# Performance work log

Measured on AMD Instinct MI355X. Metric: run time of the kernel, lower is better.

Reference implementation:

```python
import jax, jax.numpy as jnp
import numpy as np

DIM = 14                     # input feature dim == log2(codebook_size)
NUM_CODEBOOKS = 1
CODEBOOK_DIM = DIM           # codebook_dim = log2(2**dim) = dim
CODEBOOK_SIZE = 2 ** DIM     # 16384
DIVERSITY_GAMMA = 1.0
ENTROPY_LOSS_WEIGHT = 0.1
COMMITMENT_LOSS_WEIGHT = 0.25
INV_TEMPERATURE = 100.0
EPS = 1e-5


def _entropy(p):
    # -sum p log p over last dim
    return -(p * jnp.log(jnp.clip(p, EPS))).sum(-1)


def _codebook():
    # all sign codes: bit j of code i -> +/-1, MSB-first mask 2**(d-1..0)
    codes = jnp.arange(CODEBOOK_SIZE, dtype=jnp.int32)[:, None]
    shifts = jnp.arange(CODEBOOK_DIM - 1, -1, -1, dtype=jnp.int32)
    bits = (codes >> shifts) & 1                       # [cs, d]
    return (bits * 2 - 1).astype(jnp.float32)          # [cs, d]


def setup_inputs() -> dict:
    key = jax.random.key(0)
    k1, k2, k3, k4, k5 = jax.random.split(key, 5)
    b, n = 4, 2048
    cdims = CODEBOOK_DIM * NUM_CODEBOOKS
    s = 1.0 / np.sqrt(DIM)
    return {
        "x": jax.random.normal(k1, (b, n, DIM), dtype=jnp.float32),
        "W_in": jax.random.uniform(k2, (cdims, DIM), jnp.float32, -s, s),
        "b_in": jax.random.uniform(k3, (cdims,), jnp.float32, -s, s),
        "W_out": jax.random.uniform(k4, (DIM, cdims), jnp.float32, -s, s),
        "b_out": jax.random.uniform(k5, (DIM,), jnp.float32, -s, s),
    }


def reference(x, W_in, b_in, W_out, b_out):
    b, n, _ = x.shape
    codebook = _codebook()                              # [cs, d]

    h = x @ W_in.T + b_in                               # [b, n, c*d]
    h = h.reshape(b, n, NUM_CODEBOOKS, CODEBOOK_DIM)    # [b, n, c, d]
    original_input = h

    # sign quantization (codebook_scale = 1.0)
    quantized = jnp.where(h > 0, 1.0, -1.0)
    # straight-through estimator (activation = identity)
    h_st = h + jax.lax.stop_gradient(quantized - h)

    # bitmask -> integer indices, MSB-first
    bit_mask = (2 ** jnp.arange(CODEBOOK_DIM - 1, -1, -1)).astype(jnp.int32)
    indices = ((h_st > 0).astype(jnp.int32) * bit_mask).sum(-1)  # [b, n, c]

    # entropy aux loss: prob over all 2**d codes
    # -distance = 2 * <orig, code>; softmax((-distance) * inv_temp)
    logits = (2.0 * INV_TEMPERATURE) * jnp.einsum(
        "bncd,jd->bncj", original_input, codebook)      # [b, n, c, cs]
    prob = jax.nn.softmax(logits, axis=-1)
    prob_flat = prob.reshape(b * n, NUM_CODEBOOKS, CODEBOOK_SIZE)

    per_sample_entropy = _entropy(prob_flat).mean()
    avg_prob = prob_flat.mean(0)                        # [c, cs]
    codebook_entropy = _entropy(avg_prob).mean()
    entropy_aux_loss = per_sample_entropy - DIVERSITY_GAMMA * codebook_entropy

    commit_loss = jnp.mean(
        (original_input - jax.lax.stop_gradient(quantized)) ** 2)

    out = h_st.reshape(b, n, NUM_CODEBOOKS * CODEBOOK_DIM) @ W_out.T + b_out

    indices = indices.squeeze(-1)  # keep_num_codebooks_dim False (c == 1)
    aux_loss = (entropy_aux_loss * ENTROPY_LOSS_WEIGHT
                + commit_loss * COMMITMENT_LOSS_WEIGHT)
    return out, indices, aux_loss
```

## Files before the change

kernel.cpp:

```cpp
#include <hip/hip_runtime.h>
#include <hip/hip_bf16.h>

#define NS 8192
#define D 14
#define CS 16384
#define EPS 1e-5f
#define LNEPS (-11.512925464970229f)
#define THRESH 30.0f

__global__ __launch_bounds__(256) void lfq_zero(float* __restrict__ hist)
{
    ((float4*)hist)[blockIdx.x * 256 + threadIdx.x] =
        make_float4(0.f, 0.f, 0.f, 0.f);
}

__global__ __launch_bounds__(64) void lfq_main(
    const float* __restrict__ x, const float* __restrict__ Win,
    const float* __restrict__ bin, const float* __restrict__ Wout,
    const float* __restrict__ bout,
    float* __restrict__ out, float* __restrict__ idxOut,
    float* __restrict__ hist, float* __restrict__ entPart,
    float* __restrict__ commitPart)
{
    const int tid = threadIdx.x;
    const int i = blockIdx.x * 64 + tid;

    float xv[D];
    #pragma unroll
    for (int k = 0; k < D; k++) xv[k] = x[i * D + k];

    float h[D];
    #pragma unroll
    for (int d = 0; d < D; d++) {
        float s = bin[d];
        #pragma unroll
        for (int k = 0; k < D; k++) s = fmaf(xv[k], Win[d * D + k], s);
        h[d] = s;
    }

    float q[D];
    int idx = 0;
    float commit = 0.f;
    #pragma unroll
    for (int d = 0; d < D; d++) {
        const bool pos = h[d] > 0.f;
        q[d] = pos ? 1.f : -1.f;
        idx |= (pos ? 1 : 0) << (13 - d);
        const float e = h[d] - q[d];
        commit = fmaf(e, e, commit);
    }

    #pragma unroll
    for (int e = 0; e < D; e++) {
        float s = bout[e];
        #pragma unroll
        for (int d = 0; d < D; d++) s = fmaf(q[d], Wout[e * D + d], s);
        out[i * D + e] = s;
    }
    idxOut[i] = (float)idx;

    __shared__ float sA[D * 64];
    __shared__ int   sB[D * 64];
    int S = 0;
    float t0 = 0.f;
    #pragma unroll
    for (int d = 0; d < D; d++) {
        const float ab = fabsf(200.0f * h[d]);
        t0 -= __logf(1.0f + __expf(-2.f * ab));
        const float twoA = 2.f * ab;
        if (twoA < THRESH) {
            sA[S * 64 + tid] = twoA;
            sB[S * 64 + tid] = 1 << (13 - d);
            S++;
        }
    }

    float ent;
    {
        const float p0 = __expf(t0);
        ent = p0 * fmaxf(t0, LNEPS);
        atomicAdd(&hist[idx], p0);
    }
    float tcur = t0;
    int jj = idx;
    const int total = 1 << S;
    for (int m = 1; m < total; m++) {
        const int k = __ffs(m) - 1;
        const int gn = m ^ (m >> 1);
        const float tw = sA[k * 64 + tid];
        const int bm = sB[k * 64 + tid];
        tcur += ((gn >> k) & 1) ? -tw : tw;
        jj ^= bm;
        const float p = __expf(tcur);
        ent = fmaf(p, fmaxf(tcur, LNEPS), ent);
        atomicAdd(&hist[jj], p);
    }

    __shared__ float red[64];
    red[tid] = commit;
    __syncthreads();
    #pragma unroll
    for (int s = 32; s > 0; s >>= 1) {
        if (tid < s) red[tid] += red[tid + s];
        __syncthreads();
    }
    if (tid == 0) commitPart[blockIdx.x] = red[0];
    __syncthreads();
    red[tid] = ent;
    __syncthreads();
    #pragma unroll
    for (int s = 32; s > 0; s >>= 1) {
        if (tid < s) red[tid] += red[tid + s];
        __syncthreads();
    }
    if (tid == 0) entPart[blockIdx.x] = red[0];
}

__global__ __launch_bounds__(256) void lfq_r1(
    const float* __restrict__ hist, float* __restrict__ cbPart)
{
    const int t = threadIdx.x;
    const float4 v = ((const float4*)hist)[blockIdx.x * 256 + t];
    float cb = 0.f;
    #pragma unroll
    for (int u = 0; u < 4; u++) {
        const float qv = (&v.x)[u] * (1.0f / NS);
        cb += qv * __logf(fmaxf(qv, EPS));
    }
    __shared__ float r[256];
    r[t] = cb;
    __syncthreads();
    #pragma unroll
    for (int s = 128; s > 0; s >>= 1) {
        if (t < s) r[t] += r[t + s];
        __syncthreads();
    }
    if (t == 0) cbPart[blockIdx.x] = r[0];
}

__global__ __launch_bounds__(256) void lfq_r2(
    const float* __restrict__ cbPart, const float* __restrict__ entPart,
    const float* __restrict__ commitPart, float* __restrict__ aux)
{
    const int t = threadIdx.x;
    float cb = (t < 16) ? cbPart[t] : 0.f;
    float es = (t < 128) ? entPart[t] : 0.f;
    float cm = (t < 128) ? commitPart[t] : 0.f;

    __shared__ float r1[256], r2[256], r3[256];
    r1[t] = cb; r2[t] = es; r3[t] = cm;
    __syncthreads();
    #pragma unroll
    for (int s = 128; s > 0; s >>= 1) {
        if (t < s) { r1[t] += r1[t + s]; r2[t] += r2[t + s]; r3[t] += r3[t + s]; }
        __syncthreads();
    }
    if (t == 0) {
        const float codebook_entropy = -r1[0];
        const float per_sample_entropy = -r2[0] / (float)NS;
        const float commit_loss = r3[0] / (float)(NS * D);
        const float entropy_aux = per_sample_entropy - 1.0f * codebook_entropy;
        aux[0] = entropy_aux * 0.1f + commit_loss * 0.25f;
    }
}

extern "C" void kernel_launch(void* const* d_in, const int* in_sizes, int n_in,
                              void* d_out, int out_size, void* d_ws, size_t ws_size,
                              hipStream_t stream) {
    const float* x    = (const float*)d_in[0];
    const float* Win  = (const float*)d_in[1];
    const float* bin  = (const float*)d_in[2];
    const float* Wout = (const float*)d_in[3];
    const float* bout = (const float*)d_in[4];

    float* out    = (float*)d_out;
    float* idxOut = out + (size_t)NS * D;
    float* aux    = idxOut + NS;

    float* ws         = (float*)d_ws;
    float* hist       = ws;
    float* entPart    = hist + CS;
    float* commitPart = entPart + 128;
    float* cbPart     = commitPart + 128;

    lfq_zero<<<16, 256, 0, stream>>>(hist);
    lfq_main<<<NS / 64, 64, 0, stream>>>(x, Win, bin, Wout, bout,
                                         out, idxOut, hist, entPart, commitPart);
    lfq_r1<<<16, 256, 0, stream>>>(hist, cbPart);
    lfq_r2<<<1, 256, 0, stream>>>(cbPart, entPart, commitPart, aux);
}
```

Before: 27.78 us.

## Fuse four LFQ kernels into one cooperative kernel with grid syncs

Replaces the zero, main, and two reduction kernels with a single cooperative launch that zeroes the histogram, computes per-sample work, and uses grid.sync barriers before the histogram accumulation and the final reduction. Block reductions switch from shared-memory trees to wave shuffles. This removes three kernel launches and the gaps between them. In exchange, the final codebook-entropy pass over the 16K-entry histogram runs on a single 64-thread block, and the grid barriers add their own cost.

```diff
diff --git a/kernel.cpp b/kernel.cpp
--- a/kernel.cpp
+++ b/kernel.cpp
@@ -1,29 +1,38 @@
 #include <hip/hip_runtime.h>
-#include <hip/hip_bf16.h>
+#include <hip/hip_cooperative_groups.h>
+
+namespace cg = cooperative_groups;
 
 #define NS 8192
 #define D 14
 #define CS 16384
+#define NB 128
+#define BT 64
 #define EPS 1e-5f
 #define LNEPS (-11.512925464970229f)
 #define THRESH 30.0f
 
-__global__ __launch_bounds__(256) void lfq_zero(float* __restrict__ hist)
-{
-    ((float4*)hist)[blockIdx.x * 256 + threadIdx.x] =
-        make_float4(0.f, 0.f, 0.f, 0.f);
+__device__ __forceinline__ float waveRedSum(float v) {
+    #pragma unroll
+    for (int off = 32; off; off >>= 1) v += __shfl_xor(v, off);
+    return v;
 }
 
-__global__ __launch_bounds__(64) void lfq_main(
+__global__ __launch_bounds__(BT) void lfq_all(
     const float* __restrict__ x, const float* __restrict__ Win,
     const float* __restrict__ bin, const float* __restrict__ Wout,
     const float* __restrict__ bout,
     float* __restrict__ out, float* __restrict__ idxOut,
     float* __restrict__ hist, float* __restrict__ entPart,
-    float* __restrict__ commitPart)
+    float* __restrict__ commitPart, float* __restrict__ aux)
 {
+    cg::grid_group grid = cg::this_grid();
     const int tid = threadIdx.x;
-    const int i = blockIdx.x * 64 + tid;
+    const int b = blockIdx.x;
+    const int i = b * BT + tid;
+
+    atomicExch(&hist[2 * i], 0.f);
+    atomicExch(&hist[2 * i + 1], 0.f);
 
     float xv[D];
     #pragma unroll
@@ -59,8 +68,8 @@
     }
     idxOut[i] = (float)idx;
 
-    __shared__ float sA[D * 64];
-    __shared__ int   sB[D * 64];
+    __shared__ float sA[D * BT];
+    __shared__ int   sB[D * BT];
     int S = 0;
     float t0 = 0.f;
     #pragma unroll
@@ -69,11 +78,16 @@
         t0 -= __logf(1.0f + __expf(-2.f * ab));
         const float twoA = 2.f * ab;
         if (twoA < THRESH) {
-            sA[S * 64 + tid] = twoA;
-            sB[S * 64 + tid] = 1 << (13 - d);
+            sA[S * BT + tid] = twoA;
+            sB[S * BT + tid] = 1 << (13 - d);
             S++;
         }
     }
+
+    const float cm = waveRedSum(commit);
+    if (tid == 0) atomicExch(&commitPart[b], cm);
+
+    grid.sync();
 
     float ent;
     {
@@ -87,8 +101,8 @@
     for (int m = 1; m < total; m++) {
         const int k = __ffs(m) - 1;
         const int gn = m ^ (m >> 1);
-        const float tw = sA[k * 64 + tid];
-        const int bm = sB[k * 64 + tid];
+        const float tw = sA[k * BT + tid];
+        const int bm = sB[k * BT + tid];
         tcur += ((gn >> k) & 1) ? -tw : tw;
         jj ^= bm;
         const float p = __expf(tcur);
@@ -96,71 +110,34 @@
         atomicAdd(&hist[jj], p);
     }
 
-    __shared__ float red[64];
-    red[tid] = commit;
-    __syncthreads();
-    #pragma unroll
-    for (int s = 32; s > 0; s >>= 1) {
-        if (tid < s) red[tid] += red[tid + s];
-        __syncthreads();
-    }
-    if (tid == 0) commitPart[blockIdx.x] = red[0];
-    __syncthreads();
-    red[tid] = ent;
-    __syncthreads();
-    #pragma unroll
-    for (int s = 32; s > 0; s >>= 1) {
-        if (tid < s) red[tid] += red[tid + s];
-        __syncthreads();
-    }
-    if (tid == 0) entPart[blockIdx.x] = red[0];
-}
+    const float es = waveRedSum(ent);
+    if (tid == 0) atomicExch(&entPart[b], es);
 
-__global__ __launch_bounds__(256) void lfq_r1(
-    const float* __restrict__ hist, float* __restrict__ cbPart)
-{
-    const int t = threadIdx.x;
-    const float4 v = ((const float4*)hist)[blockIdx.x * 256 + t];
-    float cb = 0.f;
-    #pragma unroll
-    for (int u = 0; u < 4; u++) {
-        const float qv = (&v.x)[u] * (1.0f / NS);
-        cb += qv * __logf(fmaxf(qv, EPS));
-    }
-    __shared__ float r[256];
-    r[t] = cb;
-    __syncthreads();
-    #pragma unroll
-    for (int s = 128; s > 0; s >>= 1) {
-        if (t < s) r[t] += r[t + s];
-        __syncthreads();
-    }
-    if (t == 0) cbPart[blockIdx.x] = r[0];
-}
+    grid.sync();
 
-__global__ __launch_bounds__(256) void lfq_r2(
-    const float* __restrict__ cbPart, const float* __restrict__ entPart,
-    const float* __restrict__ commitPart, float* __restrict__ aux)
-{
-    const int t = threadIdx.x;
-    float cb = (t < 16) ? cbPart[t] : 0.f;
-    float es = (t < 128) ? entPart[t] : 0.f;
-    float cm = (t < 128) ? commitPart[t] : 0.f;
-
-    __shared__ float r1[256], r2[256], r3[256];
-    r1[t] = cb; r2[t] = es; r3[t] = cm;
-    __syncthreads();
-    #pragma unroll
-    for (int s = 128; s > 0; s >>= 1) {
-        if (t < s) { r1[t] += r1[t + s]; r2[t] += r2[t + s]; r3[t] += r3[t + s]; }
-        __syncthreads();
-    }
-    if (t == 0) {
-        const float codebook_entropy = -r1[0];
-        const float per_sample_entropy = -r2[0] / (float)NS;
-        const float commit_loss = r3[0] / (float)(NS * D);
-        const float entropy_aux = per_sample_entropy - 1.0f * codebook_entropy;
-        aux[0] = entropy_aux * 0.1f + commit_loss * 0.25f;
+    if (b == 0) {
+        float cb = 0.f;
+        const float4* h4 = (const float4*)hist;
+        for (int u = 0; u < 64; u++) {
+            const float4 v = h4[u * BT + tid];
+            #pragma unroll
+            for (int w = 0; w < 4; w++) {
+                const float qv = (&v.x)[w] * (1.0f / NS);
+                cb += qv * __logf(fmaxf(qv, EPS));
+            }
+        }
+        float es2 = entPart[tid] + entPart[tid + 64];
+        float cm2 = commitPart[tid] + commitPart[tid + 64];
+        cb  = waveRedSum(cb);
+        es2 = waveRedSum(es2);
+        cm2 = waveRedSum(cm2);
+        if (tid == 0) {
+            const float codebook_entropy = -cb;
+            const float per_sample_entropy = -es2 / (float)NS;
+            const float commit_loss = cm2 / (float)(NS * D);
+            const float entropy_aux = per_sample_entropy - 1.0f * codebook_entropy;
+            aux[0] = entropy_aux * 0.1f + commit_loss * 0.25f;
+        }
     }
 }
 
@@ -180,12 +157,13 @@
     float* ws         = (float*)d_ws;
     float* hist       = ws;
     float* entPart    = hist + CS;
-    float* commitPart = entPart + 128;
-    float* cbPart     = commitPart + 128;
+    float* commitPart = entPart + NB;
 
-    lfq_zero<<<16, 256, 0, stream>>>(hist);
-    lfq_main<<<NS / 64, 64, 0, stream>>>(x, Win, bin, Wout, bout,
-                                         out, idxOut, hist, entPart, commitPart);
-    lfq_r1<<<16, 256, 0, stream>>>(hist, cbPart);
-    lfq_r2<<<1, 256, 0, stream>>>(cbPart, entPart, commitPart, aux);
+    void* args[] = {
+        (void*)&x, (void*)&Win, (void*)&bin, (void*)&Wout, (void*)&bout,
+        (void*)&out, (void*)&idxOut, (void*)&hist, (void*)&entPart,
+        (void*)&commitPart, (void*)&aux
+    };
+    hipLaunchCooperativeKernel((const void*)lfq_all, dim3(NB), dim3(BT),
+                               args, 0, stream);
 }
```

Measured after the change: 61.73 us. 122% more time.
